# Kernel tuning notes

Hardware: AMD Instinct MI355X
Metric: run time of the kernel (lower is better)

The kernel has to match this reference:

```python
import jax, jax.numpy as jnp
import numpy as np

B, S, D, H = 2, 1024, 1024, 2048
E = 8          # hash_size: number of expert FFNs
DICT = 32000   # dict_size: vocab for the hash map


def setup_inputs() -> dict:
    key = jax.random.key(0)
    k = jax.random.split(key, 7)
    x = jax.random.normal(k[0], (B, S, D), dtype=jnp.float32)
    orig_input = jax.random.randint(k[1], (B, S), 0, DICT, dtype=jnp.int32)
    # random token -> expert hash map (random.randrange(0, hashsize) in original)
    hash_map = jax.random.randint(k[2], (DICT,), 0, E, dtype=jnp.int32)
    # torch Linear weights are [out, in]; xavier_uniform for weights, default uniform for biases
    lim1 = float(np.sqrt(6.0 / (D + H)))
    lim2 = float(np.sqrt(6.0 / (H + D)))
    W1 = jax.random.uniform(k[3], (E, H, D), minval=-lim1, maxval=lim1, dtype=jnp.float32)
    b1 = jax.random.uniform(k[4], (E, H), minval=-1.0 / np.sqrt(D), maxval=1.0 / np.sqrt(D), dtype=jnp.float32)
    W2 = jax.random.uniform(k[5], (E, D, H), minval=-lim2, maxval=lim2, dtype=jnp.float32)
    b2 = jax.random.uniform(k[6], (E, D), minval=-1.0 / np.sqrt(H), maxval=1.0 / np.sqrt(H), dtype=jnp.float32)
    return {"x": x, "orig_input": orig_input, "hash_map": hash_map,
            "W1": W1, "b1": b1, "W2": W2, "b2": b2}


def reference(x, orig_input, hash_map, W1, b1, W2, b2):
    # expert id per token (hash routing)
    e = hash_map[orig_input]                      # [B, S]
    out = jnp.zeros_like(x)
    # loop over the small fixed set of experts; each iteration is a dense
    # 2-layer FFN, with the token->expert mask selecting which outputs land.
    # (relu_dropout = 0 -> identity; eval-mode semantics)
    for i in range(E):
        h = jax.nn.relu(jnp.einsum('bsd,hd->bsh', x, W1[i]) + b1[i])   # [B,S,H]
        y = jnp.einsum('bsh,dh->bsd', h, W2[i]) + b2[i]                # [B,S,D]
        out = jnp.where((e == i)[..., None], y, out)
    return out
```

## Files before the change

### kernel.cpp

```cpp
#include <hip/hip_runtime.h>
#include <hip/hip_bf16.h>
#include <stdint.h>

#define TOKENS 2048
#define DD 1024
#define HH 2048
#define NE 8
#define RP_CAP 3072
#define BM 128
#define BN 64
#define BK 64

typedef float f32x4 __attribute__((ext_vector_type(4)));
typedef short bf16x8 __attribute__((ext_vector_type(8)));
typedef unsigned int u32;

__device__ __forceinline__ unsigned short f2bf(float f) {
    union { float f; u32 u; } v; v.f = f;
    u32 u = v.u;
    return (unsigned short)((u + 0x7fffu + ((u >> 16) & 1u)) >> 16);
}

__global__ __launch_bounds__(256) void k_route(const int* __restrict__ orig,
                                               const int* __restrict__ hmap,
                                               int* __restrict__ hdr) {
    __shared__ int s_e[TOKENS];
    __shared__ int s_cnt[NE];
    __shared__ int s_off[NE];
    int tid = threadIdx.x;
    if (tid < NE) s_cnt[tid] = 0;
    __syncthreads();
    for (int t = tid; t < TOKENS; t += 256) {
        int e = hmap[orig[t]];
        s_e[t] = e;
        atomicAdd(&s_cnt[e], 1);
    }
    __syncthreads();
    if (tid == 0) {
        int run = 0;
        for (int e = 0; e < NE; ++e) {
            s_off[e] = run;
            hdr[e] = s_cnt[e];
            hdr[8 + e] = run;
            run += ((s_cnt[e] + BM - 1) / BM) * BM;
        }
        hdr[16] = run;
    }
    __syncthreads();
    int* perm = hdr + 64;
    for (int r = tid; r < RP_CAP; r += 256) perm[r] = -1;
    if (tid < NE) s_cnt[tid] = 0;
    __syncthreads();
    for (int t = tid; t < TOKENS; t += 256) {
        int e = s_e[t];
        int pos = s_off[e] + atomicAdd(&s_cnt[e], 1);
        perm[pos] = t;
    }
}

__global__ __launch_bounds__(256) void k_gather(const float* __restrict__ x,
                                                const int* __restrict__ hdr,
                                                unsigned short* __restrict__ xp) {
    int r = blockIdx.x;
    int t = hdr[64 + r];
    int tid = threadIdx.x;
    ushort4* dst = (ushort4*)(xp + (size_t)r * DD);
    if (t >= 0) {
        const float4* src = (const float4*)(x + (size_t)t * DD);
        float4 v = src[tid];
        ushort4 o;
        o.x = f2bf(v.x); o.y = f2bf(v.y); o.z = f2bf(v.z); o.w = f2bf(v.w);
        dst[tid] = o;
    } else {
        ushort4 z; z.x = 0; z.y = 0; z.z = 0; z.w = 0;
        dst[tid] = z;
    }
}

template<int KDIM, int NDIM, bool L2EPI>
__global__ __launch_bounds__(256, 3) void k_gemm(const unsigned short* __restrict__ A,
                                                 const float* __restrict__ W,
                                                 const float* __restrict__ bias,
                                                 const int* __restrict__ hdr,
                                                 unsigned short* __restrict__ hout,
                                                 float* __restrict__ out) {
    int total = hdr[16];
    int row0 = blockIdx.y * BM;
    if (row0 >= total) return;
    int e = 0;
#pragma unroll
    for (int i = 1; i < NE; ++i)
        if (row0 >= hdr[8 + i]) e = i;

    int n0 = blockIdx.x * BN;
    const float* We = W + (size_t)e * NDIM * KDIM;
    const float* be = bias + (size_t)e * NDIM;

    __shared__ __align__(16) unsigned short As[2 * BM * BK];
    __shared__ __align__(16) unsigned short Bs[2 * BN * BK];

    int tid = threadIdx.x;
    int w = tid >> 6, lane = tid & 63;
    int wr = w >> 1, wc = w & 1;
    int fr = lane & 15, hi = lane >> 4;

    f32x4 acc[4][2];
#pragma unroll
    for (int m = 0; m < 4; ++m)
#pragma unroll
        for (int n = 0; n < 2; ++n) acc[m][n] = f32x4{0.f, 0.f, 0.f, 0.f};

    float4 bvA[4], bvB[4];

    auto STAGE_A = [&](int buf, int k0) {
#pragma unroll
        for (int j = 0; j < 4; ++j) {
            int c = j * 256 + tid;
            int row = c >> 3;
            int slot = c & 7;
            int gslot = slot ^ (row & 7);
            const unsigned short* gp = A + (size_t)(row0 + row) * KDIM + k0 + gslot * 8;
            unsigned short* lp = (unsigned short*)As + buf * (BM * BK) + j * 2048 + w * 512;
            __builtin_amdgcn_global_load_lds((const __attribute__((address_space(1))) u32*)gp,
                                             (__attribute__((address_space(3))) u32*)lp, 16, 0, 0);
        }
    };
    auto B_LOAD = [&](float4 (&bv)[4], int k0) {
#pragma unroll
        for (int jr = 0; jr < 2; ++jr) {
            int c = jr * 256 + tid;
            int row = c >> 3;
            int cl = c & 7;
            const float4* gp = (const float4*)(We + (size_t)(n0 + row) * KDIM + k0 + cl * 8);
            bv[jr * 2]     = gp[0];
            bv[jr * 2 + 1] = gp[1];
        }
    };
    auto B_WRITE = [&](const float4 (&bv)[4], int buf) {
        unsigned short* Bb = Bs + buf * (BN * BK);
#pragma unroll
        for (int jr = 0; jr < 2; ++jr) {
            int c = jr * 256 + tid;
            int row = c >> 3;
            int cl = c & 7;
            float4 v0 = bv[jr * 2], v1 = bv[jr * 2 + 1];
            union { bf16x8 v; unsigned short s[8]; } o;
            o.s[0] = f2bf(v0.x); o.s[1] = f2bf(v0.y); o.s[2] = f2bf(v0.z); o.s[3] = f2bf(v0.w);
            o.s[4] = f2bf(v1.x); o.s[5] = f2bf(v1.y); o.s[6] = f2bf(v1.z); o.s[7] = f2bf(v1.w);
            int sp = cl ^ (row & 7);
            *(bf16x8*)&Bb[row * 64 + sp * 8] = o.v;
        }
    };
    auto COMPUTE = [&](int buf) {
        const unsigned short* Ab = As + buf * (BM * BK);
        const unsigned short* Bb = Bs + buf * (BN * BK);
#pragma unroll
        for (int kk = 0; kk < BK; kk += 32) {
            bf16x8 af[4], bfr[2];
#pragma unroll
            for (int m = 0; m < 4; ++m) {
                int rr = wr * 64 + m * 16 + fr;
                int idx = (rr * 64 + kk + hi * 8) ^ ((rr & 7) << 3);
                af[m] = *(const bf16x8*)&Ab[idx];
            }
#pragma unroll
            for (int n = 0; n < 2; ++n) {
                int cn = wc * 32 + n * 16 + fr;
                int idx = (cn * 64 + kk + hi * 8) ^ ((cn & 7) << 3);
                bfr[n] = *(const bf16x8*)&Bb[idx];
            }
#pragma unroll
            for (int m = 0; m < 4; ++m)
#pragma unroll
                for (int n = 0; n < 2; ++n)
                    acc[m][n] = __builtin_amdgcn_mfma_f32_16x16x32_bf16(af[m], bfr[n], acc[m][n], 0, 0, 0);
        }
    };

    constexpr int NT = KDIM / BK;

#define WAIT_KEEP4 asm volatile("s_waitcnt vmcnt(4) lgkmcnt(0)" ::: "memory")
#define WAIT_ALL   asm volatile("s_waitcnt vmcnt(0) lgkmcnt(0)" ::: "memory")
#define BARRIER    do { __builtin_amdgcn_s_barrier(); asm volatile("" ::: "memory"); } while (0)

    STAGE_A(0, 0);
    B_LOAD(bvA, 0);
    B_LOAD(bvB, BK);
    B_WRITE(bvA, 0);
    WAIT_KEEP4;
    BARRIER;

    for (int t = 0; t < NT; t += 2) {
        STAGE_A(1, (t + 1) * BK);
        if (t + 2 < NT) B_LOAD(bvA, (t + 2) * BK);
        COMPUTE(0);
        B_WRITE(bvB, 1);
        if (t + 2 < NT) WAIT_KEEP4; else WAIT_ALL;
        BARRIER;
        if (t + 2 < NT) {
            STAGE_A(0, (t + 2) * BK);
            if (t + 3 < NT) B_LOAD(bvB, (t + 3) * BK);
            COMPUTE(1);
            B_WRITE(bvA, 0);
            if (t + 3 < NT) WAIT_KEEP4; else WAIT_ALL;
            BARRIER;
        } else {
            COMPUTE(1);
        }
    }
#undef WAIT_KEEP4
#undef WAIT_ALL
#undef BARRIER

    const int* perm = hdr + 64;
    int rbase = row0 + wr * 64 + hi * 4;
    int cbase = n0 + wc * 32 + fr;
    if constexpr (!L2EPI) {
#pragma unroll
        for (int n = 0; n < 2; ++n) {
            int cg = cbase + n * 16;
            float bvv = be[cg];
#pragma unroll
            for (int m = 0; m < 4; ++m) {
                int rg = rbase + m * 16;
#pragma unroll
                for (int r = 0; r < 4; ++r) {
                    float v = acc[m][n][r] + bvv;
                    v = v > 0.f ? v : 0.f;
                    hout[(size_t)(rg + r) * NDIM + cg] = f2bf(v);
                }
            }
        }
    } else {
        float bvv[2];
#pragma unroll
        for (int n = 0; n < 2; ++n) bvv[n] = be[cbase + n * 16];
#pragma unroll
        for (int m = 0; m < 4; ++m) {
            int rg = rbase + m * 16;
#pragma unroll
            for (int r = 0; r < 4; ++r) {
                int t = perm[rg + r];
                if (t < 0) continue;
                float* op = out + (size_t)t * DD;
#pragma unroll
                for (int n = 0; n < 2; ++n)
                    op[cbase + n * 16] = acc[m][n][r] + bvv[n];
            }
        }
    }
}

extern "C" void kernel_launch(void* const* d_in, const int* in_sizes, int n_in,
                              void* d_out, int out_size, void* d_ws, size_t ws_size,
                              hipStream_t stream) {
    const float* x    = (const float*)d_in[0];
    const int*   orig = (const int*)d_in[1];
    const int*   hmap = (const int*)d_in[2];
    const float* W1   = (const float*)d_in[3];
    const float* b1   = (const float*)d_in[4];
    const float* W2   = (const float*)d_in[5];
    const float* b2   = (const float*)d_in[6];
    float* out = (float*)d_out;

    int* hdr = (int*)d_ws;
    unsigned short* xp   = (unsigned short*)((char*)d_ws + 16384);
    unsigned short* hbuf = (unsigned short*)((char*)d_ws + 16384 + (size_t)RP_CAP * DD * 2);

    k_route<<<1, 256, 0, stream>>>(orig, hmap, hdr);
    k_gather<<<RP_CAP, 256, 0, stream>>>(x, hdr, xp);
    k_gemm<DD, HH, false><<<dim3(HH / BN, RP_CAP / BM), 256, 0, stream>>>(xp, W1, b1, hdr, hbuf, nullptr);
    k_gemm<HH, DD, true><<<dim3(DD / BN, RP_CAP / BM), 256, 0, stream>>>(hbuf, W2, b2, hdr, nullptr, out);
}
```

Before: 78.35 us.

## Triple-buffer A/B shared tiles to prefetch A two stages ahead

Grows the LDS ring for the A and B GEMM tiles from two stages to three, so asynchronous A tile loads are issued two k-steps ahead, and lowers the occupancy hint from 3 to 2 blocks per CU. The main loop now rotates buffer offsets, waits with vmcnt(8) and uses sched_barrier to keep more global loads in flight. This aims to hide global memory latency better, at the cost of more LDS per block and possibly fewer resident waves.

```diff
diff --git a/kernel.cpp b/kernel.cpp
--- a/kernel.cpp
+++ b/kernel.cpp
@@ -78,7 +78,7 @@
 }
 
 template<int KDIM, int NDIM, bool L2EPI>
-__global__ __launch_bounds__(256, 3) void k_gemm(const unsigned short* __restrict__ A,
+__global__ __launch_bounds__(256, 2) void k_gemm(const unsigned short* __restrict__ A,
                                                  const float* __restrict__ W,
                                                  const float* __restrict__ bias,
                                                  const int* __restrict__ hdr,
@@ -96,8 +96,8 @@
     const float* We = W + (size_t)e * NDIM * KDIM;
     const float* be = bias + (size_t)e * NDIM;
 
-    __shared__ __align__(16) unsigned short As[2 * BM * BK];
-    __shared__ __align__(16) unsigned short Bs[2 * BN * BK];
+    __shared__ __align__(16) unsigned short As[3 * BM * BK];
+    __shared__ __align__(16) unsigned short Bs[3 * BN * BK];
 
     int tid = threadIdx.x;
     int w = tid >> 6, lane = tid & 63;
@@ -112,7 +112,7 @@
 
     float4 bvA[4], bvB[4];
 
-    auto STAGE_A = [&](int buf, int k0) {
+    auto STAGE_A = [&](int aoff, int k0) {
 #pragma unroll
         for (int j = 0; j < 4; ++j) {
             int c = j * 256 + tid;
@@ -120,7 +120,7 @@
             int slot = c & 7;
             int gslot = slot ^ (row & 7);
             const unsigned short* gp = A + (size_t)(row0 + row) * KDIM + k0 + gslot * 8;
-            unsigned short* lp = (unsigned short*)As + buf * (BM * BK) + j * 2048 + w * 512;
+            unsigned short* lp = (unsigned short*)As + aoff + j * 2048 + w * 512;
             __builtin_amdgcn_global_load_lds((const __attribute__((address_space(1))) u32*)gp,
                                              (__attribute__((address_space(3))) u32*)lp, 16, 0, 0);
         }
@@ -136,8 +136,8 @@
             bv[jr * 2 + 1] = gp[1];
         }
     };
-    auto B_WRITE = [&](const float4 (&bv)[4], int buf) {
-        unsigned short* Bb = Bs + buf * (BN * BK);
+    auto B_WRITE = [&](const float4 (&bv)[4], int boff) {
+        unsigned short* Bb = Bs + boff;
 #pragma unroll
         for (int jr = 0; jr < 2; ++jr) {
             int c = jr * 256 + tid;
@@ -151,9 +151,9 @@
             *(bf16x8*)&Bb[row * 64 + sp * 8] = o.v;
         }
     };
-    auto COMPUTE = [&](int buf) {
-        const unsigned short* Ab = As + buf * (BM * BK);
-        const unsigned short* Bb = Bs + buf * (BN * BK);
+    auto COMPUTE = [&](int aoff, int boff) {
+        const unsigned short* Ab = As + aoff;
+        const unsigned short* Bb = Bs + boff;
 #pragma unroll
         for (int kk = 0; kk < BK; kk += 32) {
             bf16x8 af[4], bfr[2];
@@ -179,37 +179,50 @@
 
     constexpr int NT = KDIM / BK;
 
-#define WAIT_KEEP4 asm volatile("s_waitcnt vmcnt(4) lgkmcnt(0)" ::: "memory")
-#define WAIT_ALL   asm volatile("s_waitcnt vmcnt(0) lgkmcnt(0)" ::: "memory")
-#define BARRIER    do { __builtin_amdgcn_s_barrier(); asm volatile("" ::: "memory"); } while (0)
-
-    STAGE_A(0, 0);
+#define WAIT8   do { asm volatile("s_waitcnt vmcnt(8) lgkmcnt(0)" ::: "memory"); \
+                     __builtin_amdgcn_sched_barrier(0); } while (0)
+#define WAIT0   do { asm volatile("s_waitcnt vmcnt(0) lgkmcnt(0)" ::: "memory"); \
+                     __builtin_amdgcn_sched_barrier(0); } while (0)
+#define BARRIER do { __builtin_amdgcn_s_barrier(); asm volatile("" ::: "memory"); } while (0)
+
+    constexpr int ASZ = BM * BK;
+    constexpr int BSZ = BN * BK;
+    int a0 = 0, a1 = ASZ, a2 = 2 * ASZ;
+    int b0 = 0, b1 = BSZ, b2 = 2 * BSZ;
+
+    STAGE_A(a0, 0);
     B_LOAD(bvA, 0);
+    STAGE_A(a1, BK);
     B_LOAD(bvB, BK);
-    B_WRITE(bvA, 0);
-    WAIT_KEEP4;
+    B_WRITE(bvA, b0);
+    WAIT8;
     BARRIER;
 
-    for (int t = 0; t < NT; t += 2) {
-        STAGE_A(1, (t + 1) * BK);
-        if (t + 2 < NT) B_LOAD(bvA, (t + 2) * BK);
-        COMPUTE(0);
-        B_WRITE(bvB, 1);
-        if (t + 2 < NT) WAIT_KEEP4; else WAIT_ALL;
+    for (int t = 0; t + 3 < NT; t += 2) {
+        STAGE_A(a2, (t + 2) * BK);
+        B_LOAD(bvA, (t + 2) * BK);
+        COMPUTE(a0, b0);
+        B_WRITE(bvB, b1);
+        WAIT8;
         BARRIER;
-        if (t + 2 < NT) {
-            STAGE_A(0, (t + 2) * BK);
-            if (t + 3 < NT) B_LOAD(bvB, (t + 3) * BK);
-            COMPUTE(1);
-            B_WRITE(bvA, 0);
-            if (t + 3 < NT) WAIT_KEEP4; else WAIT_ALL;
-            BARRIER;
-        } else {
-            COMPUTE(1);
-        }
-    }
-#undef WAIT_KEEP4
-#undef WAIT_ALL
+        STAGE_A(a0, (t + 3) * BK);
+        B_LOAD(bvB, (t + 3) * BK);
+        COMPUTE(a1, b1);
+        B_WRITE(bvA, b2);
+        WAIT8;
+        BARRIER;
+        int ta = a0; a0 = a2; a2 = a1; a1 = ta;
+        int tb = b0; b0 = b2; b2 = b1; b1 = tb;
+    }
+
+    COMPUTE(a0, b0);
+    B_WRITE(bvB, b1);
+    WAIT0;
+    BARRIER;
+    COMPUTE(a1, b1);
+
+#undef WAIT8
+#undef WAIT0
 #undef BARRIER
 
     const int* perm = hdr + 64;
```

After: 91.05 us. +16.2%, slower.
